# Performance work log

Hardware: AMD Instinct MI355X
Metric: run time of the kernel (lower is better)

Reference implementation:

```python
import jax, jax.numpy as jnp
import numpy as np
import math

N_HEADS = 16
EMBED = 1024
D_KEY = EMBED // N_HEADS
B, S = 2, 2048
NEG = -1000000000.0


def setup_inputs() -> dict:
    key = jax.random.key(0)
    ks = jax.random.split(key, 7)
    scale = 1.0 / math.sqrt(EMBED)
    x = jax.random.normal(ks[0], (B, S, EMBED), dtype=jnp.float32)
    Wq_w = jax.random.uniform(ks[1], (EMBED, EMBED), jnp.float32, -scale, scale)
    Wq_b = jax.random.uniform(ks[2], (EMBED,), jnp.float32, -scale, scale)
    Wk_w = jax.random.uniform(ks[3], (EMBED, EMBED), jnp.float32, -scale, scale)
    Wk_b = jax.random.uniform(ks[4], (EMBED,), jnp.float32, -scale, scale)
    Wv_w = jax.random.uniform(ks[5], (EMBED, EMBED), jnp.float32, -scale, scale)
    Wv_b = jax.random.uniform(ks[6], (EMBED,), jnp.float32, -scale, scale)
    return {"x": x, "Wq_w": Wq_w, "Wq_b": Wq_b, "Wk_w": Wk_w, "Wk_b": Wk_b,
            "Wv_w": Wv_w, "Wv_b": Wv_b, "is_masked": 1}


def reference(x, Wq_w, Wq_b, Wk_w, Wk_b, Wv_w, Wv_b, is_masked):
    b, s, e = x.shape
    # nn.Linear: y = x @ W.T + b
    q = x @ Wq_w.T + Wq_b
    k = x @ Wk_w.T + Wk_b
    v = x @ Wv_w.T + Wv_b
    # [B, H, S, Dk]
    q = q.reshape(b, s, N_HEADS, D_KEY).transpose(0, 2, 1, 3)
    k = k.reshape(b, s, N_HEADS, D_KEY).transpose(0, 2, 1, 3)
    v = v.reshape(b, s, N_HEADS, D_KEY).transpose(0, 2, 1, 3)
    scores = jnp.einsum("bhqd,bhkd->bhqk", q, k) / math.sqrt(D_KEY)
    # non-standard mask: keep positions where score != padding (0)
    mask = scores != 0.0
    if is_masked:
        causal = jnp.tril(jnp.ones((1, s, s), dtype=bool))  # broadcasts over B,H
        mask = causal[None] & mask  # [1,1,S,S] & [B,H,S,S]
    scores = jnp.where(mask, scores, NEG)
    probs = jax.nn.softmax(scores, axis=-1)
    out = jnp.einsum("bhqk,bhkd->bhqd", probs, v)
    return out.transpose(0, 2, 1, 3).reshape(b, s, e)
```

## Files before the change

kernel.cpp:

```cpp
#include <hip/hip_runtime.h>

#define B_SZ   2
#define NH     16
#define S_LEN  2048
#define DK     64
#define EMB    1024
#define M_TOT  (B_SZ * S_LEN)
#define KT     64

typedef float          f32x4  __attribute__((ext_vector_type(4)));
typedef float          f32x16 __attribute__((ext_vector_type(16)));
typedef unsigned int   u32x4  __attribute__((ext_vector_type(4)));
typedef unsigned short u16x8  __attribute__((ext_vector_type(8)));
typedef unsigned short u16x4  __attribute__((ext_vector_type(4)));
typedef __bf16         bf16x8 __attribute__((ext_vector_type(8)));

static __device__ __forceinline__ f32x4 mfma16(u16x8 a, u16x8 b, f32x4 c) {
    return __builtin_amdgcn_mfma_f32_16x16x32_bf16(
        __builtin_bit_cast(bf16x8, a), __builtin_bit_cast(bf16x8, b), c, 0, 0, 0);
}
static __device__ __forceinline__ f32x16 mfma32(u16x8 a, u16x8 b, f32x16 c) {
    return __builtin_amdgcn_mfma_f32_32x32x16_bf16(
        __builtin_bit_cast(bf16x8, a), __builtin_bit_cast(bf16x8, b), c, 0, 0, 0);
}

static __device__ __forceinline__ unsigned short f2bf(float f) {
    unsigned int u = __builtin_bit_cast(unsigned int, f);
    u = (u + 0x7FFFu + ((u >> 16) & 1u)) >> 16;
    return (unsigned short)u;
}

static __device__ __forceinline__ float exp2_hw(float x) {
    float r; asm("v_exp_f32 %0, %1" : "=v"(r) : "v"(x)); return r;
}

static __device__ __forceinline__ void barrier_raw() {
    asm volatile("s_barrier" ::: "memory");
}
#define VMCNT8() asm volatile("s_waitcnt vmcnt(8)" ::: "memory")
#define VMCNT4() asm volatile("s_waitcnt vmcnt(4)" ::: "memory")
#define VMCNT0() asm volatile("s_waitcnt vmcnt(0)" ::: "memory")

#define GLDS16(g, l)  __builtin_amdgcn_global_load_lds(                      \
    (const void __attribute__((address_space(1)))*)(g),                      \
    (void __attribute__((address_space(3)))*)(l), 16, 0, 0)

__global__ __launch_bounds__(256) void cvt_kernel(
    const float* __restrict__ x,  const float* __restrict__ wq,
    const float* __restrict__ wk, const float* __restrict__ wv,
    unsigned short* __restrict__ xb,  unsigned short* __restrict__ wqb,
    unsigned short* __restrict__ wkb, unsigned short* __restrict__ wvb)
{
    long gid = (long)blockIdx.x * 256 + threadIdx.x;
    long e = gid * 4;
    const float* src; unsigned short* dst; long off;
    if      (e < 4194304L) { src = x;  dst = xb;  off = e; }
    else if (e < 5242880L) { src = wq; dst = wqb; off = e - 4194304L; }
    else if (e < 6291456L) { src = wk; dst = wkb; off = e - 5242880L; }
    else                   { src = wv; dst = wvb; off = e - 6291456L; }
    f32x4 v = *(const f32x4*)(src + off);
    u16x4 u;
    u[0] = f2bf(v[0]); u[1] = f2bf(v[1]); u[2] = f2bf(v[2]); u[3] = f2bf(v[3]);
    *(u16x4*)(dst + off) = u;
}

__global__ __launch_bounds__(512) void qkv_gemm(
    const unsigned short* __restrict__ xb,
    const unsigned short* __restrict__ wb,
    const float* __restrict__ bq, const float* __restrict__ bk,
    const float* __restrict__ bv,
    unsigned short* __restrict__ qkv)
{
    const int tid  = threadIdx.x;
    const int lane = tid & 63;
    const int wid  = tid >> 6;
    const int wm   = wid >> 2, wn = wid & 3;
    const int n0   = blockIdx.x * 256;
    const int m0   = blockIdx.y * 256;
    const int l15  = lane & 15;
    const int k4   = lane >> 4;

    __shared__ __align__(16) unsigned short Al[4][256 * 32];
    __shared__ __align__(16) unsigned short Bl[4][256 * 32];

    f32x4 acc[8][4];
#pragma unroll
    for (int i = 0; i < 8; ++i)
#pragma unroll
        for (int j = 0; j < 4; ++j)
            acc[i][j] = (f32x4){0.f, 0.f, 0.f, 0.f};

    const int row0 = tid >> 2, row1 = (512 + tid) >> 2;
    const int sl   = tid & 3;
    const int c0   = (sl ^ (row0 & 3)) << 3;
    const int c1   = (sl ^ (row1 & 3)) << 3;
    const int d0   = (wid * 64) * 8;
    const int d1   = (512 + wid * 64) * 8;
    const unsigned short* gA0 = xb + (size_t)(m0 + row0) * EMB + c0;
    const unsigned short* gA1 = xb + (size_t)(m0 + row1) * EMB + c1;
    const unsigned short* gB0 = wb + (size_t)(n0 + row0) * EMB + c0;
    const unsigned short* gB1 = wb + (size_t)(n0 + row1) * EMB + c1;

#define STAGE_A(kt, b) do {                                     \
        GLDS16(gA0 + (kt) * 32, &Al[b][d0]);                    \
        GLDS16(gA1 + (kt) * 32, &Al[b][d1]); } while (0)
#define STAGE_B(kt, b) do {                                     \
        GLDS16(gB0 + (kt) * 32, &Bl[b][d0]);                    \
        GLDS16(gB1 + (kt) * 32, &Bl[b][d1]); } while (0)

    const int rsl = (k4 ^ (l15 & 3)) << 3;
    const int abase = wm * 128 + l15;
    const int bbase = wn * 64 + l15;

    STAGE_A(0, 0); STAGE_B(0, 0);
    STAGE_A(1, 1); STAGE_B(1, 1);
    STAGE_A(2, 2); STAGE_B(2, 2);
    VMCNT8();
    barrier_raw();

    for (int kt = 0; kt < 32; ++kt) {
        const int b = kt & 3;
        const unsigned short* Ab = Al[b];
        const unsigned short* Bb = Bl[b];

        u16x8 bfr[4], afr[4];
#pragma unroll
        for (int j = 0; j < 4; ++j)
            bfr[j] = *(const u16x8*)&Bb[(bbase + j * 16) * 32 + rsl];
#pragma unroll
        for (int i = 0; i < 4; ++i)
            afr[i] = *(const u16x8*)&Ab[(abase + i * 16) * 32 + rsl];
        if (kt + 3 < 32) STAGE_A(kt + 3, (kt + 3) & 3);
        __builtin_amdgcn_s_setprio(1);
#pragma unroll
        for (int i = 0; i < 4; ++i)
#pragma unroll
            for (int j = 0; j < 4; ++j)
                acc[i][j] = mfma16(afr[i], bfr[j], acc[i][j]);
        __builtin_amdgcn_s_setprio(0);
        barrier_raw();

#pragma unroll
        for (int i = 0; i < 4; ++i)
            afr[i] = *(const u16x8*)&Ab[(abase + (4 + i) * 16) * 32 + rsl];
        if (kt + 3 < 32) STAGE_B(kt + 3, (kt + 3) & 3);
        __builtin_amdgcn_s_setprio(1);
#pragma unroll
        for (int i = 0; i < 4; ++i)
#pragma unroll
            for (int j = 0; j < 4; ++j)
                acc[4 + i][j] = mfma16(afr[i], bfr[j], acc[4 + i][j]);
        __builtin_amdgcn_s_setprio(0);

        if (kt == 29)      VMCNT4();
        else if (kt == 30) VMCNT0();
        else               VMCNT8();
        barrier_raw();
    }

    const int mat = n0 >> 10;
    const float* bias = (mat == 0) ? bq : ((mat == 1) ? bk : bv);
    unsigned short* dst = qkv + (size_t)mat * ((size_t)M_TOT * EMB);
    const int nb = (n0 & 1023) + wn * 64;
#pragma unroll
    for (int fc = 0; fc < 4; ++fc) {
        const int nl = nb + fc * 16 + l15;
        const float bvv = bias[nl];
        const int h = nl >> 6, d = nl & 63;
#pragma unroll
        for (int fr = 0; fr < 8; ++fr) {
#pragma unroll
            for (int rr = 0; rr < 4; ++rr) {
                const int m = m0 + wm * 128 + fr * 16 + k4 * 4 + rr;
                const int bb = m >> 11, s = m & 2047;
                dst[((size_t)((bb * NH + h) * S_LEN + s)) * DK + d] =
                    f2bf(acc[fr][fc][rr] + bvv);
            }
        }
    }
#undef STAGE_A
#undef STAGE_B
}

__global__ __launch_bounds__(512) void attn_kernel(
    const unsigned short* __restrict__ Q,
    const unsigned short* __restrict__ K,
    const unsigned short* __restrict__ V,
    const int* __restrict__ mskp,
    float* __restrict__ out)
{
    const int tid = threadIdx.x, lane = tid & 63, wid = tid >> 6;
    const int grp = wid >> 2, qw = wid & 3;
    const int l31 = lane & 31, H = lane >> 5;
    const int bh = blockIdx.x;
    const int h  = bh & 15, b = bh >> 4;
    const int y  = blockIdx.y;
    const int qt = (y < 8) ? y : 23 - y;
    const int q0 = qt * 128;
    const size_t hoff = ((size_t)(b * NH + h)) * S_LEN * DK;
    const unsigned short* Qh = Q + hoff;
    const unsigned short* Kh = K + hoff;
    const unsigned short* Vh = V + hoff;
    const int msk = *mskp;
    const int ntiles = msk ? (2 * qt + 2) : (S_LEN / KT);
    const int niter  = ntiles >> 1;

    __shared__ __align__(16) unsigned short Kl[2][2][64 * 64];
    __shared__ __align__(16) unsigned short Vt[2][2][64 * 64];
    __shared__ float MLbuf[512];

    const int qrow = q0 + qw * 32 + l31;
    u16x8 qf[4];
#pragma unroll
    for (int ks = 0; ks < 4; ++ks)
        qf[ks] = *(const u16x8*)(Qh + (size_t)qrow * DK + ks * 16 + H * 8);

    u16x8 ones1;
#pragma unroll
    for (int i = 0; i < 8; ++i) ones1[i] = 0x3F80;

    f32x16 o0, o1, lacc;
#pragma unroll
    for (int i = 0; i < 16; ++i) { o0[i] = 0.f; o1[i] = 0.f; lacc[i] = 0.f; }
    float mx = -1e30f;

    const int gt  = tid & 255;
    const int sr0 = gt >> 3, sc8 = gt & 7, sr1 = sr0 + 32;
    const int kwo0 = sr0 * 64 + ((sc8 ^ (sr0 & 7)) << 3);
    const int kwo1 = sr1 * 64 + ((sc8 ^ (sr1 & 7)) << 3);
    const int vwo0 = (((sr0 >> 3) ^ sc8) << 3) + (sr0 & 7);
    const int vwo1 = (((sr1 >> 3) ^ sc8) << 3) + (sr1 & 7);

    const int qmin = q0 + qw * 32;
    const int dsw0 = l31 >> 3, dsw1 = 4 + (l31 >> 3);
    const int rsw  = l31 & 7;
    const float SC2 = 0.125f * 1.4426950408889634f;

    u16x8 kr[2], vr[2];
    {
        const unsigned short* K0 = Kh + (size_t)grp * KT * DK;
        const unsigned short* V0 = Vh + (size_t)grp * KT * DK;
        kr[0] = *(const u16x8*)(K0 + (size_t)sr0 * DK + sc8 * 8);
        vr[0] = *(const u16x8*)(V0 + (size_t)sr0 * DK + sc8 * 8);
        kr[1] = *(const u16x8*)(K0 + (size_t)sr1 * DK + sc8 * 8);
        vr[1] = *(const u16x8*)(V0 + (size_t)sr1 * DK + sc8 * 8);
        unsigned short* Kg = Kl[grp][0];
        unsigned short* Vg = Vt[grp][0];
        *(u16x8*)&Kg[kwo0] = kr[0];
        *(u16x8*)&Kg[kwo1] = kr[1];
#pragma unroll
        for (int e = 0; e < 8; ++e) {
            Vg[(sc8 * 8 + e) * 64 + vwo0] = vr[0][e];
            Vg[(sc8 * 8 + e) * 64 + vwo1] = vr[1][e];
        }
        if (grp + 2 < ntiles) {
            const unsigned short* Kn = Kh + (size_t)(grp + 2) * KT * DK;
            const unsigned short* Vn = Vh + (size_t)(grp + 2) * KT * DK;
            kr[0] = *(const u16x8*)(Kn + (size_t)sr0 * DK + sc8 * 8);
            vr[0] = *(const u16x8*)(Vn + (size_t)sr0 * DK + sc8 * 8);
            kr[1] = *(const u16x8*)(Kn + (size_t)sr1 * DK + sc8 * 8);
            vr[1] = *(const u16x8*)(Vn + (size_t)sr1 * DK + sc8 * 8);
        }
    }
    __syncthreads();

    int cur = 0;
    for (int it = 0; it < niter; ++it) {
        const int kt = 2 * it + grp;

        if (kt + 2 < ntiles) {
            unsigned short* Kg = Kl[grp][cur ^ 1];
            unsigned short* Vg = Vt[grp][cur ^ 1];
            *(u16x8*)&Kg[kwo0] = kr[0];
            *(u16x8*)&Kg[kwo1] = kr[1];
#pragma unroll
            for (int e = 0; e < 8; ++e) {
                Vg[(sc8 * 8 + e) * 64 + vwo0] = vr[0][e];
                Vg[(sc8 * 8 + e) * 64 + vwo1] = vr[1][e];
            }
        }
        if (kt + 4 < ntiles) {
            const unsigned short* Kn = Kh + (size_t)(kt + 4) * KT * DK;
            const unsigned short* Vn = Vh + (size_t)(kt + 4) * KT * DK;
            kr[0] = *(const u16x8*)(Kn + (size_t)sr0 * DK + sc8 * 8);
            vr[0] = *(const u16x8*)(Vn + (size_t)sr0 * DK + sc8 * 8);
            kr[1] = *(const u16x8*)(Kn + (size_t)sr1 * DK + sc8 * 8);
            vr[1] = *(const u16x8*)(Vn + (size_t)sr1 * DK + sc8 * 8);
        }

        if (!(msk && kt * KT > qmin + 31)) {
            const unsigned short* Kg = Kl[grp][cur];
            const unsigned short* Vg = Vt[grp][cur];

            f32x16 st0, st1;
#pragma unroll
            for (int i = 0; i < 16; ++i) { st0[i] = 0.f; st1[i] = 0.f; }
            __builtin_amdgcn_s_setprio(1);
#pragma unroll
            for (int ks = 0; ks < 4; ++ks) {
                const int g = (((ks << 1) + H) ^ rsw) << 3;
                u16x8 kf0 = *(const u16x8*)&Kg[l31 * 64 + g];
                u16x8 kf1 = *(const u16x8*)&Kg[(32 + l31) * 64 + g];
                st0 = mfma32(kf0, qf[ks], st0);
                st1 = mfma32(kf1, qf[ks], st1);
            }
            __builtin_amdgcn_s_setprio(0);

            st0 *= SC2;
            st1 *= SC2;
            float p[32];
#pragma unroll
            for (int r = 0; r < 16; ++r) { p[r] = st0[r]; p[16 + r] = st1[r]; }
            const bool needmask = msk && (kt * KT + 63 > qrow);
            if (needmask) {
#pragma unroll
                for (int r = 0; r < 16; ++r) {
                    const int krow = (r & 3) + 8 * (r >> 2) + 4 * H;
                    if (kt * KT + krow > qrow)      p[r]      = -1e30f;
                    if (kt * KT + 32 + krow > qrow) p[16 + r] = -1e30f;
                }
            }

            float t8[8];
#pragma unroll
            for (int i = 0; i < 8; ++i)
                t8[i] = fmaxf(fmaxf(p[i], p[i + 8]), fmaxf(p[i + 16], p[i + 24]));
#pragma unroll
            for (int i = 0; i < 4; ++i) t8[i] = fmaxf(t8[i], t8[i + 4]);
            float mt = fmaxf(fmaxf(t8[0], t8[1]), fmaxf(t8[2], t8[3]));
            mt = fmaxf(mt, __shfl_xor(mt, 32, 64));

            if (!__all(mt <= mx + 11.54f)) {
                const float mn = fmaxf(mx, mt);
                const float al = exp2_hw(mx - mn);
                mx = mn;
                o0 *= al; o1 *= al;
                lacc[0] *= al;
            }

#pragma unroll
            for (int r = 0; r < 32; ++r) p[r] = exp2_hw(p[r] - mx);

            __builtin_amdgcn_s_setprio(1);
#pragma unroll
            for (int ks = 0; ks < 4; ++ks) {
                const int bb = ks * 8;
                unsigned int wa, wb2, wc, wd;
                asm("v_cvt_pk_bf16_f32 %0, %1, %2" : "=v"(wa)  : "v"(p[bb + 0]), "v"(p[bb + 1]));
                asm("v_cvt_pk_bf16_f32 %0, %1, %2" : "=v"(wb2) : "v"(p[bb + 2]), "v"(p[bb + 3]));
                asm("v_cvt_pk_bf16_f32 %0, %1, %2" : "=v"(wc)  : "v"(p[bb + 4]), "v"(p[bb + 5]));
                asm("v_cvt_pk_bf16_f32 %0, %1, %2" : "=v"(wd)  : "v"(p[bb + 6]), "v"(p[bb + 7]));
                asm volatile("v_permlane32_swap_b32 %0, %1" : "+v"(wa),  "+v"(wc));
                asm volatile("v_permlane32_swap_b32 %0, %1" : "+v"(wb2), "+v"(wd));
                u32x4 wv; wv[0] = wa; wv[1] = wb2; wv[2] = wc; wv[3] = wd;
                const u16x8 pb = __builtin_bit_cast(u16x8, wv);
                const int kg = (ks << 1) + H;
                u16x8 vf0 = *(const u16x8*)&Vg[l31 * 64        + ((kg ^ dsw0) << 3)];
                u16x8 vf1 = *(const u16x8*)&Vg[(32 + l31) * 64 + ((kg ^ dsw1) << 3)];
                o0 = mfma32(vf0, pb, o0);
                o1 = mfma32(vf1, pb, o1);
                lacc = mfma32(ones1, pb, lacc);
            }
            __builtin_amdgcn_s_setprio(0);
        }

        __syncthreads();
        cur ^= 1;
    }

    const int idx = qw * 64 + lane;
    float* MO = (float*)Kl + idx * 32;
    const float lsum = lacc[0];
    if (grp == 1) {
#pragma unroll
        for (int i = 0; i < 16; ++i) {
            MO[(i + idx) & 31]      = o0[i];
            MO[(16 + i + idx) & 31] = o1[i];
        }
        MLbuf[idx * 2]     = mx;
        MLbuf[idx * 2 + 1] = lsum;
    }
    __syncthreads();
    if (grp == 0) {
        const float m2 = MLbuf[idx * 2], l2 = MLbuf[idx * 2 + 1];
        const float mn = fmaxf(mx, m2);
        const float ea = exp2_hw(mx - mn);
        const float eb = exp2_hw(m2 - mn);
        const float inv = 1.f / (lsum * ea + l2 * eb);
        float* orow = out + ((size_t)(b * S_LEN) + qrow) * EMB + h * DK;
#pragma unroll
        for (int g = 0; g < 4; ++g) {
            f32x4 w0, w1;
#pragma unroll
            for (int i = 0; i < 4; ++i) {
                w0[i] = (o0[4 * g + i] * ea + MO[(4 * g + i + idx) & 31] * eb) * inv;
                w1[i] = (o1[4 * g + i] * ea + MO[(16 + 4 * g + i + idx) & 31] * eb) * inv;
            }
            *(f32x4*)&orow[8 * g + 4 * H]      = w0;
            *(f32x4*)&orow[32 + 8 * g + 4 * H] = w1;
        }
    }
}

extern "C" void kernel_launch(void* const* d_in, const int* in_sizes, int n_in,
                              void* d_out, int out_size, void* d_ws, size_t ws_size,
                              hipStream_t stream)
{
    const float* x  = (const float*)d_in[0];
    const float* wq = (const float*)d_in[1];
    const float* bq = (const float*)d_in[2];
    const float* wk = (const float*)d_in[3];
    const float* bk = (const float*)d_in[4];
    const float* wv = (const float*)d_in[5];
    const float* bv = (const float*)d_in[6];
    const int* msk  = (const int*)d_in[7];
    float* out = (float*)d_out;

    unsigned short* xb  = (unsigned short*)d_ws;
    unsigned short* wb  = xb + (size_t)M_TOT * EMB;
    unsigned short* qkv = wb + (size_t)3 * 1024 * 1024;

    cvt_kernel<<<7168, 256, 0, stream>>>(x, wq, wk, wv,
                                         xb, wb, wb + 1024 * 1024, wb + 2 * 1024 * 1024);
    qkv_gemm<<<dim3(12, 16, 1), 512, 0, stream>>>(xb, wb, bq, bk, bv, qkv);
    attn_kernel<<<dim3(32, 16, 1), 512, 0, stream>>>(
        qkv, qkv + (size_t)M_TOT * EMB, qkv + (size_t)2 * M_TOT * EMB, msk, out);
}
```

Measured before the change: 88.63 us.

## Split attention KV across four wave groups with 64-row query tiles

Attention blocks now cover 64 query rows instead of 128, and the KV tiles are split four ways across groups of two waves, not two ways across groups of four. Partial softmax states are merged in shared memory with a two-level tree reduction. The grid doubles, and the causal load-balancing pairing of query tiles is dropped. Row sums now come from a scalar accumulation instead of an extra ones-MFMA, and double buffering is replaced by single-buffered tiles with two barriers per iteration. That cuts per-block causal imbalance and adds parallelism, at the cost of more sync and extra reduction steps.

```diff
diff --git a/kernel.cpp b/kernel.cpp
--- a/kernel.cpp
+++ b/kernel.cpp
@@ -190,199 +190,212 @@
     float* __restrict__ out)
 {
     const int tid = threadIdx.x, lane = tid & 63, wid = tid >> 6;
-    const int grp = wid >> 2, qw = wid & 3;
+    const int grp = wid >> 1, qw = wid & 1;
     const int l31 = lane & 31, H = lane >> 5;
     const int bh = blockIdx.x;
     const int h  = bh & 15, b = bh >> 4;
-    const int y  = blockIdx.y;
-    const int qt = (y < 8) ? y : 23 - y;
-    const int q0 = qt * 128;
+    const int qt = blockIdx.y;
+    const int q0 = qt * 64;
     const size_t hoff = ((size_t)(b * NH + h)) * S_LEN * DK;
     const unsigned short* Qh = Q + hoff;
     const unsigned short* Kh = K + hoff;
     const unsigned short* Vh = V + hoff;
     const int msk = *mskp;
-    const int ntiles = msk ? (2 * qt + 2) : (S_LEN / KT);
-    const int niter  = ntiles >> 1;
-
-    __shared__ __align__(16) unsigned short Kl[2][2][64 * 64];
-    __shared__ __align__(16) unsigned short Vt[2][2][64 * 64];
-    __shared__ float MLbuf[512];
+    const int ntiles = msk ? (qt + 1) : (S_LEN / KT);
+    const int niter  = (ntiles + 3) >> 2;
+
+    __shared__ __align__(16) unsigned short Kl[4][64 * 64];
+    __shared__ __align__(16) unsigned short Vt[4][64 * 64];
+    __shared__ float MLbuf[768];
+    unsigned short* Kg = Kl[grp];
+    unsigned short* Vg = Vt[grp];
 
     const int qrow = q0 + qw * 32 + l31;
+    const int qmin = q0 + qw * 32;
     u16x8 qf[4];
 #pragma unroll
     for (int ks = 0; ks < 4; ++ks)
         qf[ks] = *(const u16x8*)(Qh + (size_t)qrow * DK + ks * 16 + H * 8);
 
-    u16x8 ones1;
-#pragma unroll
-    for (int i = 0; i < 8; ++i) ones1[i] = 0x3F80;
-
-    f32x16 o0, o1, lacc;
-#pragma unroll
-    for (int i = 0; i < 16; ++i) { o0[i] = 0.f; o1[i] = 0.f; lacc[i] = 0.f; }
-    float mx = -1e30f;
-
-    const int gt  = tid & 255;
-    const int sr0 = gt >> 3, sc8 = gt & 7, sr1 = sr0 + 32;
-    const int kwo0 = sr0 * 64 + ((sc8 ^ (sr0 & 7)) << 3);
-    const int kwo1 = sr1 * 64 + ((sc8 ^ (sr1 & 7)) << 3);
-    const int vwo0 = (((sr0 >> 3) ^ sc8) << 3) + (sr0 & 7);
-    const int vwo1 = (((sr1 >> 3) ^ sc8) << 3) + (sr1 & 7);
-
-    const int qmin = q0 + qw * 32;
+    f32x16 o0, o1;
+#pragma unroll
+    for (int i = 0; i < 16; ++i) { o0[i] = 0.f; o1[i] = 0.f; }
+    float mx = -1e30f, lsum = 0.f;
+
+    const int gt  = tid & 127;
+    const int sc8 = gt & 7;
+    const int rb  = gt >> 3;
+    int kwo[4], vwo[4];
+#pragma unroll
+    for (int j = 0; j < 4; ++j) {
+        const int rj = j * 16 + rb;
+        kwo[j] = rj * 64 + ((sc8 ^ (rb & 7)) << 3);
+        vwo[j] = (((rj >> 3) ^ sc8) << 3) + (rj & 7);
+    }
+
     const int dsw0 = l31 >> 3, dsw1 = 4 + (l31 >> 3);
     const int rsw  = l31 & 7;
     const float SC2 = 0.125f * 1.4426950408889634f;
-
-    u16x8 kr[2], vr[2];
-    {
-        const unsigned short* K0 = Kh + (size_t)grp * KT * DK;
-        const unsigned short* V0 = Vh + (size_t)grp * KT * DK;
-        kr[0] = *(const u16x8*)(K0 + (size_t)sr0 * DK + sc8 * 8);
-        vr[0] = *(const u16x8*)(V0 + (size_t)sr0 * DK + sc8 * 8);
-        kr[1] = *(const u16x8*)(K0 + (size_t)sr1 * DK + sc8 * 8);
-        vr[1] = *(const u16x8*)(V0 + (size_t)sr1 * DK + sc8 * 8);
-        unsigned short* Kg = Kl[grp][0];
-        unsigned short* Vg = Vt[grp][0];
-        *(u16x8*)&Kg[kwo0] = kr[0];
-        *(u16x8*)&Kg[kwo1] = kr[1];
-#pragma unroll
-        for (int e = 0; e < 8; ++e) {
-            Vg[(sc8 * 8 + e) * 64 + vwo0] = vr[0][e];
-            Vg[(sc8 * 8 + e) * 64 + vwo1] = vr[1][e];
-        }
-        if (grp + 2 < ntiles) {
-            const unsigned short* Kn = Kh + (size_t)(grp + 2) * KT * DK;
-            const unsigned short* Vn = Vh + (size_t)(grp + 2) * KT * DK;
-            kr[0] = *(const u16x8*)(Kn + (size_t)sr0 * DK + sc8 * 8);
-            vr[0] = *(const u16x8*)(Vn + (size_t)sr0 * DK + sc8 * 8);
-            kr[1] = *(const u16x8*)(Kn + (size_t)sr1 * DK + sc8 * 8);
-            vr[1] = *(const u16x8*)(Vn + (size_t)sr1 * DK + sc8 * 8);
-        }
-    }
+    const int idx  = qw * 64 + lane;
+
+    u16x8 kr[4], vr[4];
+#pragma unroll
+    for (int j = 0; j < 4; ++j) {
+        const size_t ro = ((size_t)grp * KT + j * 16 + rb) * DK + sc8 * 8;
+        kr[j] = *(const u16x8*)(Kh + ro);
+        vr[j] = *(const u16x8*)(Vh + ro);
+    }
+
+    for (int it = 0; it < niter; ++it) {
+        const int kt = 4 * it + grp;
+        const bool act = kt < ntiles;
+        __syncthreads();
+        if (act) {
+#pragma unroll
+            for (int j = 0; j < 4; ++j) {
+                *(u16x8*)&Kg[kwo[j]] = kr[j];
+#pragma unroll
+                for (int e = 0; e < 8; ++e)
+                    Vg[(sc8 * 8 + e) * 64 + vwo[j]] = vr[j][e];
+            }
+        }
+        __syncthreads();
+
+        if (kt + 4 < ntiles) {
+#pragma unroll
+            for (int j = 0; j < 4; ++j) {
+                const size_t ro = ((size_t)(kt + 4) * KT + j * 16 + rb) * DK + sc8 * 8;
+                kr[j] = *(const u16x8*)(Kh + ro);
+                vr[j] = *(const u16x8*)(Vh + ro);
+            }
+        }
+
+        if (!act || (msk && kt * KT > qmin + 31)) continue;
+
+        f32x16 st0, st1;
+#pragma unroll
+        for (int i = 0; i < 16; ++i) { st0[i] = 0.f; st1[i] = 0.f; }
+        __builtin_amdgcn_s_setprio(1);
+#pragma unroll
+        for (int ks = 0; ks < 4; ++ks) {
+            const int g = (((ks << 1) + H) ^ rsw) << 3;
+            u16x8 kf0 = *(const u16x8*)&Kg[l31 * 64 + g];
+            u16x8 kf1 = *(const u16x8*)&Kg[(32 + l31) * 64 + g];
+            st0 = mfma32(kf0, qf[ks], st0);
+            st1 = mfma32(kf1, qf[ks], st1);
+        }
+        __builtin_amdgcn_s_setprio(0);
+
+        st0 *= SC2;
+        st1 *= SC2;
+        float p[32];
+#pragma unroll
+        for (int r = 0; r < 16; ++r) { p[r] = st0[r]; p[16 + r] = st1[r]; }
+        const bool needmask = msk && (kt * KT + 63 > qrow);
+        if (needmask) {
+#pragma unroll
+            for (int r = 0; r < 16; ++r) {
+                const int krow = (r & 3) + 8 * (r >> 2) + 4 * H;
+                if (kt * KT + krow > qrow)      p[r]      = -1e30f;
+                if (kt * KT + 32 + krow > qrow) p[16 + r] = -1e30f;
+            }
+        }
+
+        float t8[8];
+#pragma unroll
+        for (int i = 0; i < 8; ++i)
+            t8[i] = fmaxf(fmaxf(p[i], p[i + 8]), fmaxf(p[i + 16], p[i + 24]));
+#pragma unroll
+        for (int i = 0; i < 4; ++i) t8[i] = fmaxf(t8[i], t8[i + 4]);
+        float mt = fmaxf(fmaxf(t8[0], t8[1]), fmaxf(t8[2], t8[3]));
+        mt = fmaxf(mt, __shfl_xor(mt, 32, 64));
+
+        if (!__all(mt <= mx + 11.54f)) {
+            const float mn = fmaxf(mx, mt);
+            const float al = exp2_hw(mx - mn);
+            mx = mn;
+            lsum *= al;
+            o0 *= al; o1 *= al;
+        }
+
+        float s8[8];
+#pragma unroll
+        for (int i = 0; i < 8; ++i) s8[i] = 0.f;
+#pragma unroll
+        for (int r = 0; r < 32; ++r) {
+            p[r] = exp2_hw(p[r] - mx);
+            s8[r & 7] += p[r];
+        }
+        float ls = ((s8[0] + s8[1]) + (s8[2] + s8[3])) +
+                   ((s8[4] + s8[5]) + (s8[6] + s8[7]));
+        ls += __shfl_xor(ls, 32, 64);
+        lsum += ls;
+
+        __builtin_amdgcn_s_setprio(1);
+#pragma unroll
+        for (int ks = 0; ks < 4; ++ks) {
+            const int bb = ks * 8;
+            unsigned int wa, wb2, wc, wd;
+            asm("v_cvt_pk_bf16_f32 %0, %1, %2" : "=v"(wa)  : "v"(p[bb + 0]), "v"(p[bb + 1]));
+            asm("v_cvt_pk_bf16_f32 %0, %1, %2" : "=v"(wb2) : "v"(p[bb + 2]), "v"(p[bb + 3]));
+            asm("v_cvt_pk_bf16_f32 %0, %1, %2" : "=v"(wc)  : "v"(p[bb + 4]), "v"(p[bb + 5]));
+            asm("v_cvt_pk_bf16_f32 %0, %1, %2" : "=v"(wd)  : "v"(p[bb + 6]), "v"(p[bb + 7]));
+            asm volatile("v_permlane32_swap_b32 %0, %1" : "+v"(wa),  "+v"(wc));
+            asm volatile("v_permlane32_swap_b32 %0, %1" : "+v"(wb2), "+v"(wd));
+            u32x4 wv; wv[0] = wa; wv[1] = wb2; wv[2] = wc; wv[3] = wd;
+            const u16x8 pb = __builtin_bit_cast(u16x8, wv);
+            const int kg = (ks << 1) + H;
+            u16x8 vf0 = *(const u16x8*)&Vg[l31 * 64        + ((kg ^ dsw0) << 3)];
+            u16x8 vf1 = *(const u16x8*)&Vg[(32 + l31) * 64 + ((kg ^ dsw1) << 3)];
+            o0 = mfma32(vf0, pb, o0);
+            o1 = mfma32(vf1, pb, o1);
+        }
+        __builtin_amdgcn_s_setprio(0);
+    }
+
     __syncthreads();
-
-    int cur = 0;
-    for (int it = 0; it < niter; ++it) {
-        const int kt = 2 * it + grp;
-
-        if (kt + 2 < ntiles) {
-            unsigned short* Kg = Kl[grp][cur ^ 1];
-            unsigned short* Vg = Vt[grp][cur ^ 1];
-            *(u16x8*)&Kg[kwo0] = kr[0];
-            *(u16x8*)&Kg[kwo1] = kr[1];
-#pragma unroll
-            for (int e = 0; e < 8; ++e) {
-                Vg[(sc8 * 8 + e) * 64 + vwo0] = vr[0][e];
-                Vg[(sc8 * 8 + e) * 64 + vwo1] = vr[1][e];
-            }
-        }
-        if (kt + 4 < ntiles) {
-            const unsigned short* Kn = Kh + (size_t)(kt + 4) * KT * DK;
-            const unsigned short* Vn = Vh + (size_t)(kt + 4) * KT * DK;
-            kr[0] = *(const u16x8*)(Kn + (size_t)sr0 * DK + sc8 * 8);
-            vr[0] = *(const u16x8*)(Vn + (size_t)sr0 * DK + sc8 * 8);
-            kr[1] = *(const u16x8*)(Kn + (size_t)sr1 * DK + sc8 * 8);
-            vr[1] = *(const u16x8*)(Vn + (size_t)sr1 * DK + sc8 * 8);
-        }
-
-        if (!(msk && kt * KT > qmin + 31)) {
-            const unsigned short* Kg = Kl[grp][cur];
-            const unsigned short* Vg = Vt[grp][cur];
-
-            f32x16 st0, st1;
-#pragma unroll
-            for (int i = 0; i < 16; ++i) { st0[i] = 0.f; st1[i] = 0.f; }
-            __builtin_amdgcn_s_setprio(1);
-#pragma unroll
-            for (int ks = 0; ks < 4; ++ks) {
-                const int g = (((ks << 1) + H) ^ rsw) << 3;
-                u16x8 kf0 = *(const u16x8*)&Kg[l31 * 64 + g];
-                u16x8 kf1 = *(const u16x8*)&Kg[(32 + l31) * 64 + g];
-                st0 = mfma32(kf0, qf[ks], st0);
-                st1 = mfma32(kf1, qf[ks], st1);
-            }
-            __builtin_amdgcn_s_setprio(0);
-
-            st0 *= SC2;
-            st1 *= SC2;
-            float p[32];
-#pragma unroll
-            for (int r = 0; r < 16; ++r) { p[r] = st0[r]; p[16 + r] = st1[r]; }
-            const bool needmask = msk && (kt * KT + 63 > qrow);
-            if (needmask) {
-#pragma unroll
-                for (int r = 0; r < 16; ++r) {
-                    const int krow = (r & 3) + 8 * (r >> 2) + 4 * H;
-                    if (kt * KT + krow > qrow)      p[r]      = -1e30f;
-                    if (kt * KT + 32 + krow > qrow) p[16 + r] = -1e30f;
-                }
-            }
-
-            float t8[8];
-#pragma unroll
-            for (int i = 0; i < 8; ++i)
-                t8[i] = fmaxf(fmaxf(p[i], p[i + 8]), fmaxf(p[i + 16], p[i + 24]));
-#pragma unroll
-            for (int i = 0; i < 4; ++i) t8[i] = fmaxf(t8[i], t8[i + 4]);
-            float mt = fmaxf(fmaxf(t8[0], t8[1]), fmaxf(t8[2], t8[3]));
-            mt = fmaxf(mt, __shfl_xor(mt, 32, 64));
-
-            if (!__all(mt <= mx + 11.54f)) {
-                const float mn = fmaxf(mx, mt);
-                const float al = exp2_hw(mx - mn);
-                mx = mn;
-                o0 *= al; o1 *= al;
-                lacc[0] *= al;
-            }
-
-#pragma unroll
-            for (int r = 0; r < 32; ++r) p[r] = exp2_hw(p[r] - mx);
-
-            __builtin_amdgcn_s_setprio(1);
-#pragma unroll
-            for (int ks = 0; ks < 4; ++ks) {
-                const int bb = ks * 8;
-                unsigned int wa, wb2, wc, wd;
-                asm("v_cvt_pk_bf16_f32 %0, %1, %2" : "=v"(wa)  : "v"(p[bb + 0]), "v"(p[bb + 1]));
-                asm("v_cvt_pk_bf16_f32 %0, %1, %2" : "=v"(wb2) : "v"(p[bb + 2]), "v"(p[bb + 3]));
-                asm("v_cvt_pk_bf16_f32 %0, %1, %2" : "=v"(wc)  : "v"(p[bb + 4]), "v"(p[bb + 5]));
-                asm("v_cvt_pk_bf16_f32 %0, %1, %2" : "=v"(wd)  : "v"(p[bb + 6]), "v"(p[bb + 7]));
-                asm volatile("v_permlane32_swap_b32 %0, %1" : "+v"(wa),  "+v"(wc));
-                asm volatile("v_permlane32_swap_b32 %0, %1" : "+v"(wb2), "+v"(wd));
-                u32x4 wv; wv[0] = wa; wv[1] = wb2; wv[2] = wc; wv[3] = wd;
-                const u16x8 pb = __builtin_bit_cast(u16x8, wv);
-                const int kg = (ks << 1) + H;
-                u16x8 vf0 = *(const u16x8*)&Vg[l31 * 64        + ((kg ^ dsw0) << 3)];
-                u16x8 vf1 = *(const u16x8*)&Vg[(32 + l31) * 64 + ((kg ^ dsw1) << 3)];
-                o0 = mfma32(vf0, pb, o0);
-                o1 = mfma32(vf1, pb, o1);
-                lacc = mfma32(ones1, pb, lacc);
-            }
-            __builtin_amdgcn_s_setprio(0);
-        }
-
-        __syncthreads();
-        cur ^= 1;
-    }
-
-    const int idx = qw * 64 + lane;
-    float* MO = (float*)Kl + idx * 32;
-    const float lsum = lacc[0];
-    if (grp == 1) {
+    if (grp == 1 || grp == 3) {
+        float* MO = ((grp == 1) ? (float*)Kl : (float*)Vt) + idx * 32;
 #pragma unroll
         for (int i = 0; i < 16; ++i) {
             MO[(i + idx) & 31]      = o0[i];
             MO[(16 + i + idx) & 31] = o1[i];
         }
-        MLbuf[idx * 2]     = mx;
-        MLbuf[idx * 2 + 1] = lsum;
+        float* ML = MLbuf + (grp == 1 ? 0 : 256);
+        ML[idx * 2]     = mx;
+        ML[idx * 2 + 1] = lsum;
+    }
+    __syncthreads();
+    if (grp == 0 || grp == 2) {
+        const float* MO = ((grp == 0) ? (float*)Kl : (float*)Vt) + idx * 32;
+        const float* ML = MLbuf + (grp == 0 ? 0 : 256);
+        const float m2 = ML[idx * 2], l2 = ML[idx * 2 + 1];
+        const float mn = fmaxf(mx, m2);
+        const float ea = exp2_hw(mx - mn);
+        const float eb = exp2_hw(m2 - mn);
+        mx = mn;
+        lsum = lsum * ea + l2 * eb;
+#pragma unroll
+        for (int i = 0; i < 16; ++i) {
+            o0[i] = o0[i] * ea + MO[(i + idx) & 31] * eb;
+            o1[i] = o1[i] * ea + MO[(16 + i + idx) & 31] * eb;
+        }
+    }
+    __syncthreads();
+    if (grp == 2) {
+        float* MO = (float*)Kl + idx * 32;
+#pragma unroll
+        for (int i = 0; i < 16; ++i) {
+            MO[(i + idx) & 31]      = o0[i];
+            MO[(16 + i + idx) & 31] = o1[i];
+        }
+        MLbuf[512 + idx * 2]     = mx;
+        MLbuf[512 + idx * 2 + 1] = lsum;
     }
     __syncthreads();
     if (grp == 0) {
-        const float m2 = MLbuf[idx * 2], l2 = MLbuf[idx * 2 + 1];
+        const float* MO = (float*)Kl + idx * 32;
+        const float m2 = MLbuf[512 + idx * 2], l2 = MLbuf[512 + idx * 2 + 1];
         const float mn = fmaxf(mx, m2);
         const float ea = exp2_hw(mx - mn);
         const float eb = exp2_hw(m2 - mn);
@@ -423,6 +436,6 @@
     cvt_kernel<<<7168, 256, 0, stream>>>(x, wq, wk, wv,
                                          xb, wb, wb + 1024 * 1024, wb + 2 * 1024 * 1024);
     qkv_gemm<<<dim3(12, 16, 1), 512, 0, stream>>>(xb, wb, bq, bk, bv, qkv);
-    attn_kernel<<<dim3(32, 16, 1), 512, 0, stream>>>(
+    attn_kernel<<<dim3(32, 32, 1), 512, 0, stream>>>(
         qkv, qkv + (size_t)M_TOT * EMB, qkv + (size_t)2 * M_TOT * EMB, msk, out);
 }
```

Result: slower. 111.4 us (+25.6%).
